# Performance work log

Hardware: AMD Instinct MI355X
Metric: run time of the kernel (lower is better)

Reference implementation:

```python
import jax, jax.numpy as jnp
import numpy as np

B = 16384          # graphs (batch)
MAX_NODES = 20     # max nodes per graph
D = 64             # node_embed_dim
DM = 128           # d_model
H = 8              # num_heads
DH = DM // H       # depth per head
SD = 64            # state_embed_dim
N = B * MAX_NODES  # total node rows


def setup_inputs() -> dict:
    key = jax.random.key(0)
    ks = jax.random.split(key, 10)
    node_embed = jax.random.normal(ks[0], (N, D), jnp.float32)
    start_idx = jax.random.randint(ks[1], (B,), 0, N)
    end_idx = jax.random.randint(ks[2], (B,), 0, N)
    # graph id of each node row (agg_state_param = per-graph sum)
    seg_ids = jnp.arange(N, dtype=jnp.int32) // MAX_NODES
    # slots are padding (sparse matmul yields zero rows there) -> idx = -1
    valid = jax.random.uniform(ks[3], (N,)) > 0.2
    pad_idx = jnp.where(valid, jnp.arange(N, dtype=jnp.int32), -1)
    s = 0.05
    Wq = jax.random.normal(ks[4], (3 * D, DM), jnp.float32) * s
    Wk = jax.random.normal(ks[5], (D, DM), jnp.float32) * s
    Wv = jax.random.normal(ks[6], (D, DM), jnp.float32) * s
    Wo = jax.random.normal(ks[7], (DM, SD), jnp.float32) * s
    bq = jnp.zeros((DM,), jnp.float32)
    bk = jnp.zeros((DM,), jnp.float32)
    bv = jnp.zeros((DM,), jnp.float32)
    bo = jnp.zeros((SD,), jnp.float32)
    return {"node_embed": node_embed, "start_idx": start_idx, "end_idx": end_idx,
            "seg_ids": seg_ids, "pad_idx": pad_idx,
            "Wq": Wq, "bq": bq, "Wk": Wk, "bk": bk,
            "Wv": Wv, "bv": bv, "Wo": Wo, "bo": bo}


def reference(node_embed, start_idx, end_idx, seg_ids, pad_idx,
              Wq, bq, Wk, bk, Wv, bv, Wo, bo):
    # sparse one-hot selections -> gathers
    start = node_embed[start_idx]                                  # [B, D]
    end = node_embed[end_idx]                                      # [B, D]
    # agg_state_param -> per-graph sum (segment reduce)
    agg = jax.ops.segment_sum(node_embed, seg_ids, num_segments=B)  # [B, D]
    raw = jnp.concatenate([agg, start, end], axis=1)               # [B, 3D]
    # dropout is identity at inference (training=False)

    # pad_node_param -> gather with zero rows for padded slots
    ok = (pad_idx >= 0)
    nodes = jnp.where(ok[:, None],
                      node_embed[jnp.clip(pad_idx, 0)], 0.0)
    nodes = nodes.reshape(B, MAX_NODES, D)                          # [B, M, D]

    # create_padding_mask: rows whose embedding sums to 0 are padding
    mask = (jnp.sum(nodes, -1) == 0).astype(nodes.dtype)            # [B, M]
    mask = mask[:, None, None, :]                                   # [B,1,1,M]

    q = (raw @ Wq + bq).reshape(B, H, 1, DH)                        # [B,H,1,dh]
    k = (nodes @ Wk + bk).reshape(B, MAX_NODES, H, DH).transpose(0, 2, 1, 3)
    v = (nodes @ Wv + bv).reshape(B, MAX_NODES, H, DH).transpose(0, 2, 1, 3)

    scale = 1.0 / jnp.sqrt(jnp.float32(DH))
    scores = jnp.einsum('bhqd,bhkd->bhqk', q, k) * scale + mask * (-1e9)
    attn = jax.nn.softmax(scores, axis=-1)                          # [B,H,1,M]
    ctx = jnp.einsum('bhqk,bhkd->bhqd', attn, v)                    # [B,H,1,dh]
    ctx = ctx.transpose(0, 2, 1, 3).reshape(B, DM)                  # [B, DM]
    return ctx @ Wo + bo                                            # [B, SD]
```

## Files before the change

kernel.cpp:

```cpp
#include <hip/hip_runtime.h>

#define MAXN 20
#define DD 64
#define DM 128
#define NH 8
#define DH 16
#define SD 64
#define NB 4
#define NROW (NB*MAXN)
#define NPAD 68
#define QKPAD 68

typedef float f32x4 __attribute__((ext_vector_type(4)));
typedef float f32x2 __attribute__((ext_vector_type(2)));

__global__ __launch_bounds__(256) void mha_state_encoder(
    const float* __restrict__ node_embed,
    const int*   __restrict__ start_idx,
    const int*   __restrict__ end_idx,
    const int*   __restrict__ pad_idx,
    const float* __restrict__ Wq, const float* __restrict__ bq,
    const float* __restrict__ Wk, const float* __restrict__ bk,
    const float* __restrict__ Wv, const float* __restrict__ bv,
    const float* __restrict__ Wo, const float* __restrict__ bo,
    float* __restrict__ out)
{
    const int b0 = blockIdx.x * NB;
    const int t  = threadIdx.x;

    __shared__ __align__(16) float nodes[NB * MAXN * NPAD];
    __shared__ __align__(16) float pool[2176];
    __shared__ __align__(16) float rawq[NB][3 * DD];
    __shared__ __align__(16) float qv[NB * DM];
    __shared__ __align__(16) float sc[NB * NH * MAXN];
    __shared__ float qb[NB * NH];
    __shared__ __align__(16) float ctx[NB * DM];
    __shared__ float validf[NROW];

    const float* nbase = node_embed + (size_t)b0 * (MAXN * DD);

    {
        int v = t;
        #pragma unroll
        for (int k = 0; k < 5; k++, v += 256) {
            const int row = v >> 4, q = (v & 15) * 4;
            *(f32x4*)&nodes[row * NPAD + q] = *(const f32x4*)&nbase[row * DD + q];
        }
    }
    if (t < NROW) validf[t] = (pad_idx[b0 * MAXN + t] >= 0) ? 1.0f : 0.0f;
    {
        const int bb = t >> 6, c = t & 63;
        const float* pg = nbase + bb * (MAXN * DD) + c;
        float s = 0.0f;
        for (int n = 0; n < MAXN; n++) s += pg[n * DD];
        rawq[bb][c] = s;
        const int rs = start_idx[b0 + bb], re = end_idx[b0 + bb];
        rawq[bb][DD + c]     = node_embed[(size_t)rs * DD + c];
        rawq[bb][2 * DD + c] = node_embed[(size_t)re * DD + c];
    }
    __syncthreads();

    {
        const int jj = (t & 63) * 2;
        const int sg = t >> 6;
        const int i0 = sg * 48;
        f32x2 a0 = {0.f, 0.f}, a1 = a0, a2 = a0, a3 = a0;
        for (int i = 0; i < 48; i++) {
            const f32x2 wv = *(const f32x2*)&Wq[(i0 + i) * DM + jj];
            a0 += wv * rawq[0][i0 + i];
            a1 += wv * rawq[1][i0 + i];
            a2 += wv * rawq[2][i0 + i];
            a3 += wv * rawq[3][i0 + i];
        }
        *(f32x2*)&pool[(sg * NB + 0) * DM + jj] = a0;
        *(f32x2*)&pool[(sg * NB + 1) * DM + jj] = a1;
        *(f32x2*)&pool[(sg * NB + 2) * DM + jj] = a2;
        *(f32x2*)&pool[(sg * NB + 3) * DM + jj] = a3;
    }
    __syncthreads();

    {
        const int bb = t >> 7, c = t & 127;
        qv[bb * DM + c] = bq[c]
            + pool[(0 * NB + bb) * DM + c] + pool[(1 * NB + bb) * DM + c]
            + pool[(2 * NB + bb) * DM + c] + pool[(3 * NB + bb) * DM + c];
        const int o2 = t + 256;
        const int bb2 = o2 >> 7, c2 = o2 & 127;
        qv[bb2 * DM + c2] = bq[c2]
            + pool[(0 * NB + bb2) * DM + c2] + pool[(1 * NB + bb2) * DM + c2]
            + pool[(2 * NB + bb2) * DM + c2] + pool[(3 * NB + bb2) * DM + c2];
    }
    __syncthreads();

    #pragma unroll
    for (int pr = 0; pr < 2; pr++) {
        const int pp = t + pr * 256;
        const int h = pp >> 6, i = pp & 63;
        const float* wr = &Wk[i * DM + h * DH];
        const f32x4 w0 = *(const f32x4*)&wr[0];
        const f32x4 w1 = *(const f32x4*)&wr[4];
        const f32x4 w2 = *(const f32x4*)&wr[8];
        const f32x4 w3 = *(const f32x4*)&wr[12];
        #pragma unroll
        for (int bb = 0; bb < NB; bb++) {
            const float* qh = &qv[bb * DM + h * DH];
            const f32x4 q0 = *(const f32x4*)&qh[0];
            const f32x4 q1 = *(const f32x4*)&qh[4];
            const f32x4 q2 = *(const f32x4*)&qh[8];
            const f32x4 q3 = *(const f32x4*)&qh[12];
            const float s =
                  w0[0]*q0[0] + w0[1]*q0[1] + w0[2]*q0[2] + w0[3]*q0[3]
                + w1[0]*q1[0] + w1[1]*q1[1] + w1[2]*q1[2] + w1[3]*q1[3]
                + w2[0]*q2[0] + w2[1]*q2[1] + w2[2]*q2[2] + w2[3]*q2[3]
                + w3[0]*q3[0] + w3[1]*q3[1] + w3[2]*q3[2] + w3[3]*q3[3];
            pool[(bb * NH + h) * QKPAD + i] = s;
        }
    }
    if (t < NB * NH) {
        const int bb = t >> 3, h = t & 7;
        const float* qh  = &qv[bb * DM + h * DH];
        const float* bkh = &bk[h * DH];
        float s = 0.0f;
        #pragma unroll
        for (int d = 0; d < DH; d++) s += qh[d] * bkh[d];
        qb[t] = s;
    }
    __syncthreads();

    {
        const int g = t >> 3;
        const int lane8 = t & 7;
        const int bb = g >> 3;
        const float qbv = qb[g];
        const int qoff = g * QKPAD;
        const int r0 = (bb * MAXN + lane8) * NPAD;
        const int r1 = (bb * MAXN + 8 + lane8) * NPAD;
        const int r2 = (bb * MAXN + 16 + (lane8 & 3)) * NPAD;
        float s0 = 0.f, s1 = 0.f, s2 = 0.f;
        #pragma unroll
        for (int c = 0; c < 16; c++) {
            const f32x4 qk4 = *(const f32x4*)&pool[qoff + c * 4];
            const f32x4 n0  = *(const f32x4*)&nodes[r0 + c * 4];
            const f32x4 n1  = *(const f32x4*)&nodes[r1 + c * 4];
            const f32x4 n2  = *(const f32x4*)&nodes[r2 + c * 4];
            s0 += qk4[0]*n0[0] + qk4[1]*n0[1] + qk4[2]*n0[2] + qk4[3]*n0[3];
            s1 += qk4[0]*n1[0] + qk4[1]*n1[1] + qk4[2]*n1[2] + qk4[3]*n1[3];
            s2 += qk4[0]*n2[0] + qk4[1]*n2[1] + qk4[2]*n2[2] + qk4[3]*n2[3];
        }
        float v0 = (s0 + qbv) * 0.25f;
        float v1 = (s1 + qbv) * 0.25f;
        float v2 = (s2 + qbv) * 0.25f;
        if (validf[bb * MAXN + lane8] == 0.0f)      v0 -= 1.0e9f;
        if (validf[bb * MAXN + 8 + lane8] == 0.0f)  v1 -= 1.0e9f;
        sc[g * MAXN + lane8]     = v0;
        sc[g * MAXN + 8 + lane8] = v1;
        if (lane8 < 4) {
            if (validf[bb * MAXN + 16 + lane8] == 0.0f) v2 -= 1.0e9f;
            sc[g * MAXN + 16 + lane8] = v2;
        }
    }
    __syncthreads();

    if (t < NB * NH) {
        float m = -INFINITY;
        for (int n = 0; n < MAXN; n++) m = fmaxf(m, sc[t * MAXN + n]);
        float sum = 0.0f;
        for (int n = 0; n < MAXN; n++) {
            const float e = __expf(sc[t * MAXN + n] - m);
            sc[t * MAXN + n] = e;
            sum += e;
        }
        const float inv = 1.0f / sum;
        for (int n = 0; n < MAXN; n++) sc[t * MAXN + n] *= inv;
    }
    __syncthreads();

    {
        const int g = t >> 3, L = t & 7;
        const int bb = g >> 3;
        f32x4 acc0 = {0.f, 0.f, 0.f, 0.f}, acc1 = acc0;
        for (int n = 0; n < MAXN; n++) {
            const float a = sc[g * MAXN + n];
            const float* nr = &nodes[(bb * MAXN + n) * NPAD + L * 8];
            acc0 += a * *(const f32x4*)nr;
            acc1 += a * *(const f32x4*)(nr + 4);
        }
        *(f32x4*)&pool[g * QKPAD + L * 8]     = acc0;
        *(f32x4*)&pool[g * QKPAD + L * 8 + 4] = acc1;
    }
    __syncthreads();

    {
        const int j = t & 127, bbp = t >> 7;
        const int h = j >> 4;
        float a0 = bv[j], a1 = a0;
        for (int i = 0; i < DD; i++) {
            const float wv = Wv[i * DM + j];
            a0 += wv * pool[((bbp    ) * NH + h) * QKPAD + i];
            a1 += wv * pool[((bbp + 2) * NH + h) * QKPAD + i];
        }
        ctx[ bbp      * DM + j] = a0;
        ctx[(bbp + 2) * DM + j] = a1;
    }
    __syncthreads();

    {
        const int j = t & 63, sg = t >> 6;
        const int i0 = sg * 32;
        float a0 = 0.f, a1 = 0.f, a2 = 0.f, a3 = 0.f;
        for (int i = 0; i < 32; i++) {
            const float wo = Wo[(i0 + i) * SD + j];
            a0 += wo * ctx[0 * DM + i0 + i];
            a1 += wo * ctx[1 * DM + i0 + i];
            a2 += wo * ctx[2 * DM + i0 + i];
            a3 += wo * ctx[3 * DM + i0 + i];
        }
        pool[(sg * NB + 0) * SD + j] = a0;
        pool[(sg * NB + 1) * SD + j] = a1;
        pool[(sg * NB + 2) * SD + j] = a2;
        pool[(sg * NB + 3) * SD + j] = a3;
    }
    __syncthreads();

    {
        const int bb = t >> 6, j = t & 63;
        const float s = bo[j]
            + pool[(0 * NB + bb) * SD + j] + pool[(1 * NB + bb) * SD + j]
            + pool[(2 * NB + bb) * SD + j] + pool[(3 * NB + bb) * SD + j];
        out[(size_t)(b0 + bb) * SD + j] = s;
    }
}

extern "C" void kernel_launch(void* const* d_in, const int* in_sizes, int n_in,
                              void* d_out, int out_size, void* d_ws, size_t ws_size,
                              hipStream_t stream) {
    const float* node_embed = (const float*)d_in[0];
    const int*   start_idx  = (const int*)d_in[1];
    const int*   end_idx    = (const int*)d_in[2];
    const int*   pad_idx    = (const int*)d_in[4];
    const float* Wq = (const float*)d_in[5];
    const float* bq = (const float*)d_in[6];
    const float* Wk = (const float*)d_in[7];
    const float* bk = (const float*)d_in[8];
    const float* Wv = (const float*)d_in[9];
    const float* bv = (const float*)d_in[10];
    const float* Wo = (const float*)d_in[11];
    const float* bo = (const float*)d_in[12];
    float* out = (float*)d_out;

    mha_state_encoder<<<16384 / NB, 256, 0, stream>>>(
        node_embed, start_idx, end_idx, pad_idx,
        Wq, bq, Wk, bk, Wv, bv, Wo, bo, out);
}
```

Baseline: 201.4 us.

## Drop shared node tile, read nodes from global, alias LDS buffers for occupancy

Removes the shared-memory copy of each block's node rows and reads node embeddings straight from global (L1/L2-cached) memory in the score and context stages. The separate rawq/qv/sc/ctx scratch arrays are collapsed into one aliased pool2 buffer, and launch bounds now request six waves per SIMD. The aim is a much smaller LDS footprint so more blocks fit per CU and latency is hidden better. In exchange, node data is fetched repeatedly from cache instead of LDS, and the per-thread strided global reads may not coalesce well.

```diff
diff --git a/kernel.cpp b/kernel.cpp
--- a/kernel.cpp
+++ b/kernel.cpp
@@ -8,13 +8,12 @@
 #define SD 64
 #define NB 4
 #define NROW (NB*MAXN)
-#define NPAD 68
 #define QKPAD 68
 
 typedef float f32x4 __attribute__((ext_vector_type(4)));
 typedef float f32x2 __attribute__((ext_vector_type(2)));
 
-__global__ __launch_bounds__(256) void mha_state_encoder(
+__global__ __launch_bounds__(256, 6) void mha_state_encoder(
     const float* __restrict__ node_embed,
     const int*   __restrict__ start_idx,
     const int*   __restrict__ end_idx,
@@ -28,35 +27,23 @@
     const int b0 = blockIdx.x * NB;
     const int t  = threadIdx.x;
 
-    __shared__ __align__(16) float nodes[NB * MAXN * NPAD];
     __shared__ __align__(16) float pool[2176];
-    __shared__ __align__(16) float rawq[NB][3 * DD];
-    __shared__ __align__(16) float qv[NB * DM];
-    __shared__ __align__(16) float sc[NB * NH * MAXN];
+    __shared__ __align__(16) float pool2[768];
     __shared__ float qb[NB * NH];
-    __shared__ __align__(16) float ctx[NB * DM];
     __shared__ float validf[NROW];
 
     const float* nbase = node_embed + (size_t)b0 * (MAXN * DD);
 
-    {
-        int v = t;
-        #pragma unroll
-        for (int k = 0; k < 5; k++, v += 256) {
-            const int row = v >> 4, q = (v & 15) * 4;
-            *(f32x4*)&nodes[row * NPAD + q] = *(const f32x4*)&nbase[row * DD + q];
-        }
-    }
     if (t < NROW) validf[t] = (pad_idx[b0 * MAXN + t] >= 0) ? 1.0f : 0.0f;
     {
         const int bb = t >> 6, c = t & 63;
         const float* pg = nbase + bb * (MAXN * DD) + c;
         float s = 0.0f;
         for (int n = 0; n < MAXN; n++) s += pg[n * DD];
-        rawq[bb][c] = s;
+        pool2[bb * 192 + c] = s;
         const int rs = start_idx[b0 + bb], re = end_idx[b0 + bb];
-        rawq[bb][DD + c]     = node_embed[(size_t)rs * DD + c];
-        rawq[bb][2 * DD + c] = node_embed[(size_t)re * DD + c];
+        pool2[bb * 192 + DD + c]     = node_embed[(size_t)rs * DD + c];
+        pool2[bb * 192 + 2 * DD + c] = node_embed[(size_t)re * DD + c];
     }
     __syncthreads();
 
@@ -67,10 +54,10 @@
         f32x2 a0 = {0.f, 0.f}, a1 = a0, a2 = a0, a3 = a0;
         for (int i = 0; i < 48; i++) {
             const f32x2 wv = *(const f32x2*)&Wq[(i0 + i) * DM + jj];
-            a0 += wv * rawq[0][i0 + i];
-            a1 += wv * rawq[1][i0 + i];
-            a2 += wv * rawq[2][i0 + i];
-            a3 += wv * rawq[3][i0 + i];
+            a0 += wv * pool2[0 * 192 + i0 + i];
+            a1 += wv * pool2[1 * 192 + i0 + i];
+            a2 += wv * pool2[2 * 192 + i0 + i];
+            a3 += wv * pool2[3 * 192 + i0 + i];
         }
         *(f32x2*)&pool[(sg * NB + 0) * DM + jj] = a0;
         *(f32x2*)&pool[(sg * NB + 1) * DM + jj] = a1;
@@ -81,12 +68,12 @@
 
     {
         const int bb = t >> 7, c = t & 127;
-        qv[bb * DM + c] = bq[c]
+        pool2[bb * DM + c] = bq[c]
             + pool[(0 * NB + bb) * DM + c] + pool[(1 * NB + bb) * DM + c]
             + pool[(2 * NB + bb) * DM + c] + pool[(3 * NB + bb) * DM + c];
         const int o2 = t + 256;
         const int bb2 = o2 >> 7, c2 = o2 & 127;
-        qv[bb2 * DM + c2] = bq[c2]
+        pool2[bb2 * DM + c2] = bq[c2]
             + pool[(0 * NB + bb2) * DM + c2] + pool[(1 * NB + bb2) * DM + c2]
             + pool[(2 * NB + bb2) * DM + c2] + pool[(3 * NB + bb2) * DM + c2];
     }
@@ -103,7 +90,7 @@
         const f32x4 w3 = *(const f32x4*)&wr[12];
         #pragma unroll
         for (int bb = 0; bb < NB; bb++) {
-            const float* qh = &qv[bb * DM + h * DH];
+            const float* qh = &pool2[bb * DM + h * DH];
             const f32x4 q0 = *(const f32x4*)&qh[0];
             const f32x4 q1 = *(const f32x4*)&qh[4];
             const f32x4 q2 = *(const f32x4*)&qh[8];
@@ -118,7 +105,7 @@
     }
     if (t < NB * NH) {
         const int bb = t >> 3, h = t & 7;
-        const float* qh  = &qv[bb * DM + h * DH];
+        const float* qh  = &pool2[bb * DM + h * DH];
         const float* bkh = &bk[h * DH];
         float s = 0.0f;
         #pragma unroll
@@ -133,16 +120,16 @@
         const int bb = g >> 3;
         const float qbv = qb[g];
         const int qoff = g * QKPAD;
-        const int r0 = (bb * MAXN + lane8) * NPAD;
-        const int r1 = (bb * MAXN + 8 + lane8) * NPAD;
-        const int r2 = (bb * MAXN + 16 + (lane8 & 3)) * NPAD;
+        const float* nr0 = nbase + (bb * MAXN + lane8) * DD;
+        const float* nr1 = nr0 + 8 * DD;
+        const float* nr2 = nbase + (bb * MAXN + 16 + (lane8 & 3)) * DD;
         float s0 = 0.f, s1 = 0.f, s2 = 0.f;
         #pragma unroll
         for (int c = 0; c < 16; c++) {
             const f32x4 qk4 = *(const f32x4*)&pool[qoff + c * 4];
-            const f32x4 n0  = *(const f32x4*)&nodes[r0 + c * 4];
-            const f32x4 n1  = *(const f32x4*)&nodes[r1 + c * 4];
-            const f32x4 n2  = *(const f32x4*)&nodes[r2 + c * 4];
+            const f32x4 n0  = *(const f32x4*)&nr0[c * 4];
+            const f32x4 n1  = *(const f32x4*)&nr1[c * 4];
+            const f32x4 n2  = *(const f32x4*)&nr2[c * 4];
             s0 += qk4[0]*n0[0] + qk4[1]*n0[1] + qk4[2]*n0[2] + qk4[3]*n0[3];
             s1 += qk4[0]*n1[0] + qk4[1]*n1[1] + qk4[2]*n1[2] + qk4[3]*n1[3];
             s2 += qk4[0]*n2[0] + qk4[1]*n2[1] + qk4[2]*n2[2] + qk4[3]*n2[3];
@@ -152,26 +139,26 @@
         float v2 = (s2 + qbv) * 0.25f;
         if (validf[bb * MAXN + lane8] == 0.0f)      v0 -= 1.0e9f;
         if (validf[bb * MAXN + 8 + lane8] == 0.0f)  v1 -= 1.0e9f;
-        sc[g * MAXN + lane8]     = v0;
-        sc[g * MAXN + 8 + lane8] = v1;
+        pool2[g * MAXN + lane8]     = v0;
+        pool2[g * MAXN + 8 + lane8] = v1;
         if (lane8 < 4) {
             if (validf[bb * MAXN + 16 + lane8] == 0.0f) v2 -= 1.0e9f;
-            sc[g * MAXN + 16 + lane8] = v2;
+            pool2[g * MAXN + 16 + lane8] = v2;
         }
     }
     __syncthreads();
 
     if (t < NB * NH) {
         float m = -INFINITY;
-        for (int n = 0; n < MAXN; n++) m = fmaxf(m, sc[t * MAXN + n]);
+        for (int n = 0; n < MAXN; n++) m = fmaxf(m, pool2[t * MAXN + n]);
         float sum = 0.0f;
         for (int n = 0; n < MAXN; n++) {
-            const float e = __expf(sc[t * MAXN + n] - m);
-            sc[t * MAXN + n] = e;
+            const float e = __expf(pool2[t * MAXN + n] - m);
+            pool2[t * MAXN + n] = e;
             sum += e;
         }
         const float inv = 1.0f / sum;
-        for (int n = 0; n < MAXN; n++) sc[t * MAXN + n] *= inv;
+        for (int n = 0; n < MAXN; n++) pool2[t * MAXN + n] *= inv;
     }
     __syncthreads();
 
@@ -180,8 +167,8 @@
         const int bb = g >> 3;
         f32x4 acc0 = {0.f, 0.f, 0.f, 0.f}, acc1 = acc0;
         for (int n = 0; n < MAXN; n++) {
-            const float a = sc[g * MAXN + n];
-            const float* nr = &nodes[(bb * MAXN + n) * NPAD + L * 8];
+            const float a = pool2[g * MAXN + n];
+            const float* nr = nbase + (bb * MAXN + n) * DD + L * 8;
             acc0 += a * *(const f32x4*)nr;
             acc1 += a * *(const f32x4*)(nr + 4);
         }
@@ -199,8 +186,8 @@
             a0 += wv * pool[((bbp    ) * NH + h) * QKPAD + i];
             a1 += wv * pool[((bbp + 2) * NH + h) * QKPAD + i];
         }
-        ctx[ bbp      * DM + j] = a0;
-        ctx[(bbp + 2) * DM + j] = a1;
+        pool2[ bbp      * DM + j] = a0;
+        pool2[(bbp + 2) * DM + j] = a1;
     }
     __syncthreads();
 
@@ -210,10 +197,10 @@
         float a0 = 0.f, a1 = 0.f, a2 = 0.f, a3 = 0.f;
         for (int i = 0; i < 32; i++) {
             const float wo = Wo[(i0 + i) * SD + j];
-            a0 += wo * ctx[0 * DM + i0 + i];
-            a1 += wo * ctx[1 * DM + i0 + i];
-            a2 += wo * ctx[2 * DM + i0 + i];
-            a3 += wo * ctx[3 * DM + i0 + i];
+            a0 += wo * pool2[0 * DM + i0 + i];
+            a1 += wo * pool2[1 * DM + i0 + i];
+            a2 += wo * pool2[2 * DM + i0 + i];
+            a3 += wo * pool2[3 * DM + i0 + i];
         }
         pool[(sg * NB + 0) * SD + j] = a0;
         pool[(sg * NB + 1) * SD + j] = a1;
```

Result: slower. 304.9 us (+51.4%).
